# Kernel tuning notes

Measured on AMD Instinct MI355X. Metric: run time of the kernel, lower is better.

## Reference

```python
import jax, jax.numpy as jnp
import numpy as np

H = 128
N = 50000
E = 800000
VOCAB = 100
NUM_EDGE_BLOCKS = 4
NUM_UPD_BLOCKS = 2


def setup_inputs() -> dict:
    key = jax.random.key(0)
    ks = jax.random.split(key, 30)
    s = H ** -0.5
    nrm = lambda k, shp, sc: (jax.random.normal(k, shp, dtype=jnp.float32) * sc)
    inp = {
        'atom_num': jax.random.randint(ks[0], (N,), 0, VOCAB),
        'dis1': jax.random.uniform(ks[1], (E, 1), dtype=jnp.float32),
        'dis2': jax.random.uniform(ks[2], (E, 1), dtype=jnp.float32),
        'id1u': jax.random.randint(ks[3], (E,), 0, N),
        'id1v': jax.random.randint(ks[4], (E,), 0, N),
        'id2u': jax.random.randint(ks[5], (E,), 0, N),
        'id2v': jax.random.randint(ks[6], (E,), 0, N),
        # atom embedding table
        'emb': nrm(ks[7], (VOCAB, H), 1.0),
        # 4 edge-embedding blocks (edge_emb1, edge_emb2, update_edge1, update_edge2)
        'Wu': nrm(ks[8], (NUM_EDGE_BLOCKS, H, H), s),
        'Wv': nrm(ks[9], (NUM_EDGE_BLOCKS, H, H), s),
        'Wdis': nrm(ks[10], (NUM_EDGE_BLOCKS, 1, H), 1.0),
        'eb1': jnp.zeros((NUM_EDGE_BLOCKS, H), jnp.float32),
        'eW2': nrm(ks[11], (NUM_EDGE_BLOCKS, H, H), s),
        'eb2': jnp.zeros((NUM_EDGE_BLOCKS, H), jnp.float32),
        'eW3': nrm(ks[12], (NUM_EDGE_BLOCKS, H, H), s),
        'eb3': jnp.zeros((NUM_EDGE_BLOCKS, H), jnp.float32),
        # 2 atom-update blocks
        'Wh': nrm(ks[13], (NUM_UPD_BLOCKS, H, H), s),
        'Wa1': nrm(ks[14], (NUM_UPD_BLOCKS, H, H), s),
        'Wa2': nrm(ks[15], (NUM_UPD_BLOCKS, H, H), s),
        'ub1': jnp.zeros((NUM_UPD_BLOCKS, H), jnp.float32),
        'uW2': nrm(ks[16], (NUM_UPD_BLOCKS, H, H), s),
        'ub2': jnp.zeros((NUM_UPD_BLOCKS, H), jnp.float32),
        # output head
        'outW': nrm(ks[17], (H, 3), s),
        'outb': jnp.zeros((3,), jnp.float32),
    }
    return inp


def _edge_block(h, u, v, dis, Wu, Wv, Wdis, b1, W2, b2, W3, b3):
    # gather endpoint features, fuse with distance embedding, 3-layer MLP
    pre = h[u] @ Wu + h[v] @ Wv + dis @ Wdis + b1  # [E,H]
    t = jax.nn.silu(pre)
    t = jax.nn.silu(t @ W2 + b2)
    return t @ W3 + b3  # [E,H]


def _atom_update(h, m1, m2, id1u, id1v, id2u, id2v, Wh, Wa1, Wa2, b1, W2, b2):
    n = h.shape[0]
    a1 = jax.ops.segment_sum(m1, id1u, num_segments=n) + jax.ops.segment_sum(m1, id1v, num_segments=n)
    a2 = jax.ops.segment_sum(m2, id2u, num_segments=n) + jax.ops.segment_sum(m2, id2v, num_segments=n)
    t = jax.nn.silu(h @ Wh + a1 @ Wa1 + a2 @ Wa2 + b1)
    return h + t @ W2 + b2


def reference(atom_num, dis1, dis2, id1u, id1v, id2u, id2v, emb, Wu, Wv, Wdis, eb1, eW2, eb2, eW3, eb3, Wh, Wa1, Wa2, ub1, uW2, ub2, outW, outb):
    eblk = lambda i, h, u, v, d: _edge_block(h, u, v, d, Wu[i], Wv[i], Wdis[i], eb1[i], eW2[i], eb2[i], eW3[i], eb3[i])
    ablk = lambda j, h, m1, m2: _atom_update(h, m1, m2, id1u, id1v, id2u, id2v, Wh[j], Wa1[j], Wa2[j], ub1[j], uW2[j], ub2[j])
    h = emb[atom_num]  # [N,H]
    m1 = eblk(0, h, id1u, id1v, dis1)
    m2 = eblk(1, h, id2u, id2v, dis2)
    h = ablk(0, h, m1, m2)
    m1 = eblk(2, h, id1u, id1v, dis1)
    m2 = eblk(3, h, id2u, id2v, dis2)
    h = ablk(1, h, m1, m2)
    return h @ outW + outb  # [N,3]
```

## Files before the change

### kernel.cpp

```cpp
#include <hip/hip_runtime.h>

#define H 128
#define NATOM 50000
#define NEDGE 800000
#define CE (NEDGE / 2)

typedef __attribute__((ext_vector_type(8))) short short8;
typedef __attribute__((ext_vector_type(4))) float f32x4;
typedef __attribute__((ext_vector_type(4))) unsigned int uint4n;

#define MFMA16(a, b, c) __builtin_amdgcn_mfma_f32_16x16x32_bf16((a), (b), (c), 0, 0, 0)

__device__ __forceinline__ unsigned short f2b(float f) {
  unsigned int u = __float_as_uint(f);
  unsigned int r = (u + 0x7FFFu + ((u >> 16) & 1u)) >> 16;
  return (unsigned short)r;
}
__device__ __forceinline__ float b2f(unsigned short b) {
  return __uint_as_float(((unsigned int)b) << 16);
}

#if __has_builtin(__builtin_amdgcn_cvt_pk_bf16_f32)
__device__ __forceinline__ unsigned int f2b2(float lo, float hi) {
  typedef __bf16 bf16x2 __attribute__((ext_vector_type(2)));
  bf16x2 r = __builtin_amdgcn_cvt_pk_bf16_f32(lo, hi);
  union { bf16x2 v; unsigned int u; } c;
  c.v = r;
  return c.u;
}
#else
__device__ __forceinline__ unsigned int f2b2(float lo, float hi) {
  return (unsigned int)f2b(lo) | ((unsigned int)f2b(hi) << 16);
}
#endif

__device__ __forceinline__ float silu_f(float x) {
  return x * __builtin_amdgcn_rcpf(1.0f + __expf(-x));
}

struct PackSrc { const float* p[24]; };

__global__ void repack_kernel(PackSrc ps, unsigned short* __restrict__ dst) {
  const float* src = ps.p[blockIdx.x];
  unsigned short* d = dst + (size_t)blockIdx.x * 16384;
  for (int s = threadIdx.x; s < 2048; s += 256) {
    const int ct = s >> 8;
    const int kc = (s >> 6) & 3;
    const int lane = s & 63;
    const int r0 = kc * 32 + (lane >> 4) * 8;
    const int col = ct * 16 + (lane & 15);
    uint4 u;
    u.x = f2b2(src[(r0 + 0) * H + col], src[(r0 + 1) * H + col]);
    u.y = f2b2(src[(r0 + 2) * H + col], src[(r0 + 3) * H + col]);
    u.z = f2b2(src[(r0 + 4) * H + col], src[(r0 + 5) * H + col]);
    u.w = f2b2(src[(r0 + 6) * H + col], src[(r0 + 7) * H + col]);
    *(uint4*)(d + s * 8) = u;
  }
}

__global__ void embed_kernel(const int* __restrict__ atom_num, const float* __restrict__ emb,
                             unsigned short* __restrict__ h0) {
  const int idx = blockIdx.x * 256 + threadIdx.x;
  const int n = idx >> 6;
  const int c = (idx & 63) * 2;
  const float* src = emb + (size_t)atom_num[n] * H + c;
  *(unsigned int*)(h0 + (size_t)n * H + c) = f2b2(src[0], src[1]);
}

__global__ void zero_int_kernel(int4* __restrict__ p, int n4) {
  const int i = blockIdx.x * 256 + threadIdx.x;
  if (i < n4) p[i] = make_int4(0, 0, 0, 0);
}

__global__ void count_kernel(const int* __restrict__ u1, const int* __restrict__ v1,
                             const int* __restrict__ u2, const int* __restrict__ v2,
                             int* __restrict__ degU, int* __restrict__ degV) {
  const int e = blockIdx.x * 256 + threadIdx.x;
  atomicAdd(degU + u1[e], 1);
  atomicAdd(degU + NATOM + u2[e], 1);
  atomicAdd(degV + v1[e], 1);
  atomicAdd(degV + NATOM + v2[e], 1);
}

__global__ void scan_phase1(const int* __restrict__ deg, int* __restrict__ partials,
                            int ncells) {
  __shared__ int sh[256];
  const int t = threadIdx.x;
  const int base = blockIdx.x * 1024 + t * 4;
  int s = 0;
#pragma unroll
  for (int j = 0; j < 4; ++j) { const int i = base + j; if (i < ncells) s += deg[i]; }
  sh[t] = s;
  __syncthreads();
  for (int off = 128; off > 0; off >>= 1) {
    if (t < off) sh[t] += sh[t + off];
    __syncthreads();
  }
  if (t == 0) partials[blockIdx.x] = sh[0];
}

__global__ void scan_phase2(int* __restrict__ partials, int np) {
  __shared__ int sh[1024];
  const int t = threadIdx.x;
  const int v = t < np ? partials[t] : 0;
  sh[t] = v;
  __syncthreads();
  for (int off = 1; off < 1024; off <<= 1) {
    int x = 0;
    if (t >= off) x = sh[t - off];
    __syncthreads();
    sh[t] += x;
    __syncthreads();
  }
  if (t < np) partials[t] = sh[t] - v;
}

__global__ void scan_phase3(const int* __restrict__ deg, const int* __restrict__ partials,
                            int* __restrict__ start, int* __restrict__ cursor, int ncells) {
  __shared__ int sh[256];
  const int t = threadIdx.x;
  const int base = blockIdx.x * 1024 + t * 4;
  int v[4];
  int s = 0;
#pragma unroll
  for (int j = 0; j < 4; ++j) {
    const int i = base + j;
    v[j] = (i < ncells) ? deg[i] : 0;
    s += v[j];
  }
  sh[t] = s;
  __syncthreads();
  const int own = s;
  for (int off = 1; off < 256; off <<= 1) {
    int x = 0;
    if (t >= off) x = sh[t - off];
    __syncthreads();
    sh[t] += x;
    __syncthreads();
  }
  int o = partials[blockIdx.x] + sh[t] - own;
#pragma unroll
  for (int j = 0; j < 4; ++j) {
    const int i = base + j;
    if (i < ncells) {
      start[i] = o;
      cursor[i] = o;
      o += v[j];
      if (i == ncells - 1) start[ncells] = o;
    }
  }
}

__global__ void fill_fused_kernel(const int* __restrict__ u1, const int* __restrict__ v1,
                                  const float* __restrict__ dis1,
                                  const int* __restrict__ u2, const int* __restrict__ v2,
                                  const float* __restrict__ dis2,
                                  int* __restrict__ curU, int* __restrict__ curV,
                                  unsigned int* __restrict__ uvS,
                                  float* __restrict__ disS, int* __restrict__ listV,
                                  int npass) {
  const int apb = (NATOM + npass - 1) / npass;
  for (int p = 0; p < npass; ++p) {
    const int lo = p * apb, hi = lo + apb;
    for (int e = blockIdx.x * 256 + threadIdx.x; e < NEDGE; e += gridDim.x * 256) {
      int a = __builtin_nontemporal_load(u1 + e);
      if (a >= lo && a < hi) {
        const int v = __builtin_nontemporal_load(v1 + e);
        const int su = atomicAdd(curU + a, 1);
        uvS[su] = (unsigned int)a | ((unsigned int)v << 16);
        disS[su] = __builtin_nontemporal_load(dis1 + e);
        const int sv = atomicAdd(curV + v, 1);
        listV[sv] = su;
      }
      a = __builtin_nontemporal_load(u2 + e);
      if (a >= lo && a < hi) {
        const int v = __builtin_nontemporal_load(v2 + e);
        const int su = atomicAdd(curU + NATOM + a, 1);
        uvS[su] = (unsigned int)a | ((unsigned int)v << 16);
        disS[su] = __builtin_nontemporal_load(dis2 + e);
        const int sv = atomicAdd(curV + NATOM + v, 1);
        listV[sv] = su;
      }
    }
  }
}

__global__ __launch_bounds__(256, 2)
void pre_kernel(const unsigned short* __restrict__ h,
                const unsigned short* __restrict__ pWu, const unsigned short* __restrict__ pWv,
                unsigned short* __restrict__ hu, unsigned short* __restrict__ hv) {
  __shared__ __attribute__((aligned(16))) unsigned short sH[64][136];
  __shared__ __attribute__((aligned(16))) unsigned short sO[64][136];

  const int tid = threadIdx.x;
  const int wave = tid >> 6;
  const int lane = tid & 63;
  const int l15 = lane & 15;
  const int quad = lane >> 4;
  const int r0 = tid >> 4;
  const int ch = tid & 15;

  short8 wU[2][4], wV[2][4];
#pragma unroll
  for (int ct = 0; ct < 2; ++ct) {
#pragma unroll
    for (int kc = 0; kc < 4; ++kc) {
      const int off = (((wave * 2 + ct) * 4 + kc) * 64 + lane) * 8;
      wU[ct][kc] = *(const short8*)(pWu + off);
      wV[ct][kc] = *(const short8*)(pWv + off);
    }
  }

  const int n0 = blockIdx.x * 64;
#pragma unroll
  for (int it = 0; it < 4; ++it) {
    const int r = r0 + it * 16;
    int g = n0 + r; if (g >= NATOM) g = NATOM - 1;
    *(uint4*)(&sH[r][ch * 8]) = *(const uint4*)(h + (size_t)g * H + ch * 8);
  }
  __syncthreads();

  f32x4 au[4][2], av[4][2];
#pragma unroll
  for (int rt = 0; rt < 4; ++rt)
#pragma unroll
    for (int ct = 0; ct < 2; ++ct) {
      au[rt][ct] = (f32x4){0.f, 0.f, 0.f, 0.f};
      av[rt][ct] = (f32x4){0.f, 0.f, 0.f, 0.f};
    }
#pragma unroll
  for (int kc = 0; kc < 4; ++kc) {
#pragma unroll
    for (int rt = 0; rt < 4; ++rt) {
      const short8 a = *(const short8*)(&sH[rt * 16 + l15][kc * 32 + quad * 8]);
#pragma unroll
      for (int ct = 0; ct < 2; ++ct) {
        au[rt][ct] = MFMA16(a, wU[ct][kc], au[rt][ct]);
        av[rt][ct] = MFMA16(a, wV[ct][kc], av[rt][ct]);
      }
    }
  }
  __syncthreads();

#pragma unroll
  for (int rt = 0; rt < 4; ++rt) {
#pragma unroll
    for (int ct = 0; ct < 2; ++ct) {
      const int col = wave * 32 + ct * 16 + l15;
#pragma unroll
      for (int r = 0; r < 4; r += 2) {
        const int row = rt * 16 + quad * 4 + r;
        const unsigned int p = f2b2(au[rt][ct][r], au[rt][ct][r + 1]);
        sO[row][col] = (unsigned short)p;
        sO[row + 1][col] = (unsigned short)(p >> 16);
      }
    }
  }
  __syncthreads();
#pragma unroll
  for (int it = 0; it < 4; ++it) {
    const int r = r0 + it * 16;
    const int g = n0 + r;
    if (g < NATOM)
      *(uint4*)(hu + (size_t)g * H + ch * 8) = *(const uint4*)(&sO[r][ch * 8]);
  }
  __syncthreads();

#pragma unroll
  for (int rt = 0; rt < 4; ++rt) {
#pragma unroll
    for (int ct = 0; ct < 2; ++ct) {
      const int col = wave * 32 + ct * 16 + l15;
#pragma unroll
      for (int r = 0; r < 4; r += 2) {
        const int row = rt * 16 + quad * 4 + r;
        const unsigned int p = f2b2(av[rt][ct][r], av[rt][ct][r + 1]);
        sO[row][col] = (unsigned short)p;
        sO[row + 1][col] = (unsigned short)(p >> 16);
      }
    }
  }
  __syncthreads();
#pragma unroll
  for (int it = 0; it < 4; ++it) {
    const int r = r0 + it * 16;
    const int g = n0 + r;
    if (g < NATOM)
      *(uint4*)(hv + (size_t)g * H + ch * 8) = *(const uint4*)(&sO[r][ch * 8]);
  }
}

__global__ __launch_bounds__(256, 3)
void edge_kernel(const unsigned short* __restrict__ hu,
                 const unsigned short* __restrict__ hv,
                 const unsigned int* __restrict__ uv,
                 const float* __restrict__ dis,
                 const unsigned short* __restrict__ pW2, const unsigned short* __restrict__ pW3,
                 const float* __restrict__ Wdis, const float* __restrict__ bb1,
                 const float* __restrict__ bb2, const float* __restrict__ bb3,
                 unsigned short* __restrict__ msg, int eBase, int nTiles) {
  __shared__ __attribute__((aligned(16))) unsigned short sA[64][136];
  __shared__ __attribute__((aligned(16))) unsigned short sB[64][136];

  const int tid = threadIdx.x;
  const int wave = tid >> 6;
  const int lane = tid & 63;
  const int l15 = lane & 15;
  const int quad = lane >> 4;
  const int r0 = tid >> 4;
  const int ch = tid & 15;

  short8 wW2[2][4], wW3[2][4];
#pragma unroll
  for (int ct = 0; ct < 2; ++ct) {
#pragma unroll
    for (int kc = 0; kc < 4; ++kc) {
      const int off = (((wave * 2 + ct) * 4 + kc) * 64 + lane) * 8;
      wW2[ct][kc] = *(const short8*)(pW2 + off);
      wW3[ct][kc] = *(const short8*)(pW3 + off);
    }
  }
  float wd8[8], b18[8];
#pragma unroll
  for (int k = 0; k < 8; ++k) { wd8[k] = Wdis[ch * 8 + k]; b18[k] = bb1[ch * 8 + k]; }
  float vb2[2], vb3[2];
#pragma unroll
  for (int ct = 0; ct < 2; ++ct) {
    const int col = wave * 32 + ct * 16 + l15;
    vb2[ct] = bb2[col]; vb3[ct] = bb3[col];
  }

  const int stride = gridDim.x;
  int tile = blockIdx.x;

  uint4 pfU[4], pfV[4];
  float pfD[4];
  if (tile < nTiles) {
    const int e0 = eBase + tile * 64;
#pragma unroll
    for (int it = 0; it < 4; ++it) {
      const int e = e0 + r0 + it * 16;
      const unsigned int p = uv[e];
      pfU[it] = *(const uint4*)(hu + (size_t)(p & 0xFFFFu) * H + ch * 8);
      pfV[it] = *(const uint4*)(hv + (size_t)(p >> 16) * H + ch * 8);
      pfD[it] = dis[e];
    }
  }

  for (; tile < nTiles; tile += stride) {
#pragma unroll
    for (int it = 0; it < 4; ++it) {
      const int rr = r0 + it * 16;
      const float d = pfD[it];
      const unsigned int ua[4] = {pfU[it].x, pfU[it].y, pfU[it].z, pfU[it].w};
      const unsigned int va[4] = {pfV[it].x, pfV[it].y, pfV[it].z, pfV[it].w};
#pragma unroll
      for (int j = 0; j < 4; ++j) {
        const float x0 = b2f((unsigned short)ua[j]) + b2f((unsigned short)va[j]) +
                         d * wd8[2 * j] + b18[2 * j];
        const float x1 = b2f((unsigned short)(ua[j] >> 16)) + b2f((unsigned short)(va[j] >> 16)) +
                         d * wd8[2 * j + 1] + b18[2 * j + 1];
        *(unsigned int*)(&sA[rr][ch * 8 + 2 * j]) = f2b2(silu_f(x0), silu_f(x1));
      }
    }
    const int tileN = tile + stride;
    if (tileN < nTiles) {
      const int e0n = eBase + tileN * 64;
#pragma unroll
      for (int it = 0; it < 4; ++it) {
        const int e = e0n + r0 + it * 16;
        const unsigned int p = uv[e];
        pfU[it] = *(const uint4*)(hu + (size_t)(p & 0xFFFFu) * H + ch * 8);
        pfV[it] = *(const uint4*)(hv + (size_t)(p >> 16) * H + ch * 8);
        pfD[it] = dis[e];
      }
    }
    __syncthreads();

    f32x4 acc[4][2];
#pragma unroll
    for (int rt = 0; rt < 4; ++rt)
#pragma unroll
      for (int ct = 0; ct < 2; ++ct) acc[rt][ct] = (f32x4){0.f, 0.f, 0.f, 0.f};
#pragma unroll
    for (int kc = 0; kc < 4; ++kc) {
#pragma unroll
      for (int rt = 0; rt < 4; ++rt) {
        const short8 a = *(const short8*)(&sA[rt * 16 + l15][kc * 32 + quad * 8]);
#pragma unroll
        for (int ct = 0; ct < 2; ++ct) acc[rt][ct] = MFMA16(a, wW2[ct][kc], acc[rt][ct]);
      }
    }
#pragma unroll
    for (int rt = 0; rt < 4; ++rt) {
#pragma unroll
      for (int ct = 0; ct < 2; ++ct) {
        const int col = wave * 32 + ct * 16 + l15;
#pragma unroll
        for (int r = 0; r < 4; r += 2) {
          const int row = rt * 16 + quad * 4 + r;
          const unsigned int p = f2b2(silu_f(acc[rt][ct][r] + vb2[ct]),
                                      silu_f(acc[rt][ct][r + 1] + vb2[ct]));
          sB[row][col] = (unsigned short)p;
          sB[row + 1][col] = (unsigned short)(p >> 16);
        }
      }
    }
    __syncthreads();

#pragma unroll
    for (int rt = 0; rt < 4; ++rt)
#pragma unroll
      for (int ct = 0; ct < 2; ++ct) acc[rt][ct] = (f32x4){0.f, 0.f, 0.f, 0.f};
#pragma unroll
    for (int kc = 0; kc < 4; ++kc) {
#pragma unroll
      for (int rt = 0; rt < 4; ++rt) {
        const short8 a = *(const short8*)(&sB[rt * 16 + l15][kc * 32 + quad * 8]);
#pragma unroll
        for (int ct = 0; ct < 2; ++ct) acc[rt][ct] = MFMA16(a, wW3[ct][kc], acc[rt][ct]);
      }
    }
#pragma unroll
    for (int rt = 0; rt < 4; ++rt) {
#pragma unroll
      for (int ct = 0; ct < 2; ++ct) {
        const int col = wave * 32 + ct * 16 + l15;
#pragma unroll
        for (int r = 0; r < 4; r += 2) {
          const int row = rt * 16 + quad * 4 + r;
          const unsigned int p = f2b2(acc[rt][ct][r] + vb3[ct],
                                      acc[rt][ct][r + 1] + vb3[ct]);
          sA[row][col] = (unsigned short)p;
          sA[row + 1][col] = (unsigned short)(p >> 16);
        }
      }
    }
    __syncthreads();
#pragma unroll
    for (int it = 0; it < 4; ++it) {
      const int rr = r0 + it * 16;
      __builtin_nontemporal_store(*(const uint4n*)(&sA[rr][ch * 8]),
                                  (uint4n*)(msg + (size_t)(tile * 64 + rr) * H + ch * 8));
    }
    __syncthreads();
  }
}

__global__ __launch_bounds__(256)
void aggregate_kernel(const int* __restrict__ startU, const int* __restrict__ startV,
                      const int* __restrict__ listV,
                      const unsigned short* __restrict__ msg, int chunkBase, int cellBase,
                      float* __restrict__ af32, unsigned short* __restrict__ aout,
                      int isFirst, int isLast) {
  const int atom = blockIdx.x * 4 + (threadIdx.x >> 6);
  const int lane = threadIdx.x & 63;
  float ax = 0.f, ay = 0.f;
  if (!isFirst) {
    const float2 p = *(const float2*)(af32 + (size_t)atom * H + lane * 2);
    ax = p.x; ay = p.y;
  }
  const unsigned int* mp = (const unsigned int*)msg;

  const int gsu = startU[cellBase + atom];
  const int geu = startU[cellBase + atom + 1];
  int lo = gsu > chunkBase ? gsu : chunkBase;
  int hi = geu < chunkBase + CE ? geu : chunkBase + CE;
  int p = lo - chunkBase;
  const int pe = hi - chunkBase;
  for (; p + 3 < pe; p += 4) {
    unsigned int u[4];
#pragma unroll
    for (int j = 0; j < 4; ++j) u[j] = mp[(size_t)(p + j) * 64 + lane];
#pragma unroll
    for (int j = 0; j < 4; ++j) {
      ax += b2f((unsigned short)u[j]);
      ay += b2f((unsigned short)(u[j] >> 16));
    }
  }
  for (; p < pe; ++p) {
    const unsigned int u0 = mp[(size_t)p * 64 + lane];
    ax += b2f((unsigned short)u0);
    ay += b2f((unsigned short)(u0 >> 16));
  }

  const int sv = startV[cellBase + atom];
  const int ev = startV[cellBase + atom + 1];
  int i = sv;
  for (; i + 7 < ev; i += 8) {
    unsigned int d[8];
#pragma unroll
    for (int j = 0; j < 8; ++j)
      d[j] = (unsigned int)(__builtin_nontemporal_load(listV + i + j) - chunkBase);
    unsigned int u[8];
#pragma unroll
    for (int j = 0; j < 8; ++j) {
      u[j] = 0u;
      if (d[j] < (unsigned int)CE)
        u[j] = __builtin_nontemporal_load(mp + (size_t)d[j] * 64 + lane);
    }
#pragma unroll
    for (int j = 0; j < 8; ++j) {
      ax += b2f((unsigned short)u[j]);
      ay += b2f((unsigned short)(u[j] >> 16));
    }
  }
  for (; i < ev; ++i) {
    const unsigned int d = (unsigned int)(__builtin_nontemporal_load(listV + i) - chunkBase);
    if (d < (unsigned int)CE) {
      const unsigned int u0 = __builtin_nontemporal_load(mp + (size_t)d * 64 + lane);
      ax += b2f((unsigned short)u0);
      ay += b2f((unsigned short)(u0 >> 16));
    }
  }

  if (isLast) {
    *(unsigned int*)(aout + (size_t)atom * H + lane * 2) = f2b2(ax, ay);
  } else {
    *(float2*)(af32 + (size_t)atom * H + lane * 2) = make_float2(ax, ay);
  }
}

__global__ __launch_bounds__(256, 2)
void update_kernel(const unsigned short* __restrict__ hin,
                   const unsigned short* __restrict__ a1, const unsigned short* __restrict__ a2,
                   const unsigned short* __restrict__ pWh, const unsigned short* __restrict__ pWa1,
                   const unsigned short* __restrict__ pWa2, const unsigned short* __restrict__ pWo,
                   const float* __restrict__ b1, const float* __restrict__ b2,
                   unsigned short* __restrict__ hout) {
  __shared__ __attribute__((aligned(16))) unsigned short sH[64][136];
  __shared__ __attribute__((aligned(16))) unsigned short s1[64][136];
  __shared__ __attribute__((aligned(16))) unsigned short s2[64][136];

  const int tid = threadIdx.x;
  const int wave = tid >> 6;
  const int lane = tid & 63;
  const int l15 = lane & 15;
  const int quad = lane >> 4;

  short8 wWh[2][4], wW1[2][4], wW2m[2][4], wWo[2][4];
#pragma unroll
  for (int ct = 0; ct < 2; ++ct) {
#pragma unroll
    for (int kc = 0; kc < 4; ++kc) {
      const int off = (((wave * 2 + ct) * 4 + kc) * 64 + lane) * 8;
      wWh[ct][kc] = *(const short8*)(pWh + off);
      wW1[ct][kc] = *(const short8*)(pWa1 + off);
      wW2m[ct][kc] = *(const short8*)(pWa2 + off);
      wWo[ct][kc] = *(const short8*)(pWo + off);
    }
  }
  float vb1[2], vb2[2];
#pragma unroll
  for (int ct = 0; ct < 2; ++ct) {
    const int col = wave * 32 + ct * 16 + l15;
    vb1[ct] = b1[col]; vb2[ct] = b2[col];
  }

  const int n0 = blockIdx.x * 64;
#pragma unroll
  for (int it = 0; it < 4; ++it) {
    const int r = (tid >> 4) + it * 16;
    const int ch = tid & 15;
    int g = n0 + r; if (g >= NATOM) g = NATOM - 1;
    *(uint4*)(&sH[r][ch * 8]) = *(const uint4*)(hin + (size_t)g * H + ch * 8);
    *(uint4*)(&s1[r][ch * 8]) = *(const uint4*)(a1 + (size_t)g * H + ch * 8);
    *(uint4*)(&s2[r][ch * 8]) = *(const uint4*)(a2 + (size_t)g * H + ch * 8);
  }
  __syncthreads();

  f32x4 acc[4][2];
#pragma unroll
  for (int rt = 0; rt < 4; ++rt)
#pragma unroll
    for (int ct = 0; ct < 2; ++ct) acc[rt][ct] = (f32x4){0.f, 0.f, 0.f, 0.f};

#pragma unroll
  for (int kc = 0; kc < 4; ++kc) {
#pragma unroll
    for (int rt = 0; rt < 4; ++rt) {
      const short8 ah = *(const short8*)(&sH[rt * 16 + l15][kc * 32 + quad * 8]);
      const short8 aa1 = *(const short8*)(&s1[rt * 16 + l15][kc * 32 + quad * 8]);
      const short8 aa2 = *(const short8*)(&s2[rt * 16 + l15][kc * 32 + quad * 8]);
#pragma unroll
      for (int ct = 0; ct < 2; ++ct) {
        acc[rt][ct] = MFMA16(ah, wWh[ct][kc], acc[rt][ct]);
        acc[rt][ct] = MFMA16(aa1, wW1[ct][kc], acc[rt][ct]);
        acc[rt][ct] = MFMA16(aa2, wW2m[ct][kc], acc[rt][ct]);
      }
    }
  }
  __syncthreads();

#pragma unroll
  for (int rt = 0; rt < 4; ++rt) {
#pragma unroll
    for (int ct = 0; ct < 2; ++ct) {
      const int col = wave * 32 + ct * 16 + l15;
#pragma unroll
      for (int r = 0; r < 4; r += 2) {
        const int row = rt * 16 + quad * 4 + r;
        const unsigned int p = f2b2(silu_f(acc[rt][ct][r] + vb1[ct]),
                                    silu_f(acc[rt][ct][r + 1] + vb1[ct]));
        s1[row][col] = (unsigned short)p;
        s1[row + 1][col] = (unsigned short)(p >> 16);
      }
    }
  }
  __syncthreads();

#pragma unroll
  for (int rt = 0; rt < 4; ++rt)
#pragma unroll
    for (int ct = 0; ct < 2; ++ct) acc[rt][ct] = (f32x4){0.f, 0.f, 0.f, 0.f};
#pragma unroll
  for (int kc = 0; kc < 4; ++kc) {
#pragma unroll
    for (int rt = 0; rt < 4; ++rt) {
      const short8 a = *(const short8*)(&s1[rt * 16 + l15][kc * 32 + quad * 8]);
#pragma unroll
      for (int ct = 0; ct < 2; ++ct) acc[rt][ct] = MFMA16(a, wWo[ct][kc], acc[rt][ct]);
    }
  }
  __syncthreads();
#pragma unroll
  for (int rt = 0; rt < 4; ++rt) {
#pragma unroll
    for (int ct = 0; ct < 2; ++ct) {
      const int col = wave * 32 + ct * 16 + l15;
#pragma unroll
      for (int r = 0; r < 4; r += 2) {
        const int row = rt * 16 + quad * 4 + r;
        const float v0 = b2f(sH[row][col]) + acc[rt][ct][r] + vb2[ct];
        const float v1 = b2f(sH[row + 1][col]) + acc[rt][ct][r + 1] + vb2[ct];
        const unsigned int p = f2b2(v0, v1);
        s2[row][col] = (unsigned short)p;
        s2[row + 1][col] = (unsigned short)(p >> 16);
      }
    }
  }
  __syncthreads();
#pragma unroll
  for (int it = 0; it < 4; ++it) {
    const int r = (tid >> 4) + it * 16;
    const int ch = tid & 15;
    const int g = n0 + r;
    if (g < NATOM)
      *(uint4*)(hout + (size_t)g * H + ch * 8) = *(const uint4*)(&s2[r][ch * 8]);
  }
}

__global__ void out_kernel(const unsigned short* __restrict__ h,
                           const float* __restrict__ outW, const float* __restrict__ outb,
                           float* __restrict__ out) {
  const int atom = blockIdx.x * 4 + (threadIdx.x >> 6);
  const int lane = threadIdx.x & 63;
  float s0 = 0.f, s1 = 0.f, s2 = 0.f;
#pragma unroll
  for (int kk = 0; kk < 2; ++kk) {
    const int k = lane + kk * 64;
    const float hv = b2f(h[(size_t)atom * H + k]);
    s0 += hv * outW[k * 3 + 0];
    s1 += hv * outW[k * 3 + 1];
    s2 += hv * outW[k * 3 + 2];
  }
#pragma unroll
  for (int off = 32; off > 0; off >>= 1) {
    s0 += __shfl_down(s0, off);
    s1 += __shfl_down(s1, off);
    s2 += __shfl_down(s2, off);
  }
  if (lane == 0) {
    out[atom * 3 + 0] = s0 + outb[0];
    out[atom * 3 + 1] = s1 + outb[1];
    out[atom * 3 + 2] = s2 + outb[2];
  }
}

extern "C" void kernel_launch(void* const* d_in, const int* in_sizes, int n_in,
                              void* d_out, int out_size, void* d_ws, size_t ws_size,
                              hipStream_t stream) {
  const int* atom_num = (const int*)d_in[0];
  const float* dis1 = (const float*)d_in[1];
  const float* dis2 = (const float*)d_in[2];
  const int* id1u = (const int*)d_in[3];
  const int* id1v = (const int*)d_in[4];
  const int* id2u = (const int*)d_in[5];
  const int* id2v = (const int*)d_in[6];
  const float* emb = (const float*)d_in[7];
  const float* Wu = (const float*)d_in[8];
  const float* Wv = (const float*)d_in[9];
  const float* Wdis = (const float*)d_in[10];
  const float* eb1 = (const float*)d_in[11];
  const float* eW2 = (const float*)d_in[12];
  const float* eb2 = (const float*)d_in[13];
  const float* eW3 = (const float*)d_in[14];
  const float* eb3 = (const float*)d_in[15];
  const float* Wh = (const float*)d_in[16];
  const float* Wa1 = (const float*)d_in[17];
  const float* Wa2 = (const float*)d_in[18];
  const float* ub1 = (const float*)d_in[19];
  const float* uW2 = (const float*)d_in[20];
  const float* ub2 = (const float*)d_in[21];
  const float* outW = (const float*)d_in[22];
  const float* outb = (const float*)d_in[23];

  auto pad = [](size_t x) { return (x + 255) & ~(size_t)255; };
  const int N2 = 2 * NATOM;
  const int nparts = (N2 + 1023) / 1024;

  char* ws = (char*)d_ws;
  size_t off = 0;
  auto take = [&](size_t bytes) { char* p = ws + off; off += pad(bytes); return p; };
  unsigned short* pw   = (unsigned short*)take(786432);
  unsigned short* h0   = (unsigned short*)take((size_t)NATOM * H * 2);
  unsigned short* a1   = (unsigned short*)take((size_t)NATOM * H * 2);
  unsigned short* a2   = (unsigned short*)take((size_t)NATOM * H * 2);
  unsigned short* hu   = (unsigned short*)take((size_t)NATOM * H * 2);
  unsigned short* hv   = (unsigned short*)take((size_t)NATOM * H * 2);
  unsigned int* uvS    = (unsigned int*)take((size_t)2 * NEDGE * 4);
  float* disS          = (float*)take((size_t)2 * NEDGE * 4);
  int* listV           = (int*)take((size_t)2 * NEDGE * 4);
  int* startU          = (int*)take(((size_t)N2 + 1) * 4);
  int* startV          = (int*)take(((size_t)N2 + 1) * 4);
  float* af32          = (float*)take((size_t)NATOM * H * 4);
  char* ovlRegion      = ws + off;
  unsigned short* msg  = (unsigned short*)ovlRegion;
  int* degU            = (int*)ovlRegion;
  int* degV            = degU + N2;
  int* curU            = degV + N2;
  int* curV            = curU + N2;
  int* partU           = curV + N2;
  int* partV           = partU + 1024;

  PackSrc ps;
  for (int i = 0; i < 4; ++i) {
    ps.p[i] = Wu + i * 16384;
    ps.p[4 + i] = Wv + i * 16384;
    ps.p[8 + i] = eW2 + i * 16384;
    ps.p[12 + i] = eW3 + i * 16384;
  }
  for (int j = 0; j < 2; ++j) {
    ps.p[16 + j] = Wh + j * 16384;
    ps.p[18 + j] = Wa1 + j * 16384;
    ps.p[20 + j] = Wa2 + j * 16384;
    ps.p[22 + j] = uW2 + j * 16384;
  }
  repack_kernel<<<24, 256, 0, stream>>>(ps, pw);
  embed_kernel<<<12500, 256, 0, stream>>>(atom_num, emb, h0);

  {
    const int n4 = (int)(((size_t)2 * N2 * 4 + 15) / 16);
    zero_int_kernel<<<(n4 + 255) / 256, 256, 0, stream>>>((int4*)degU, n4);
    count_kernel<<<NEDGE / 256, 256, 0, stream>>>(id1u, id1v, id2u, id2v, degU, degV);
    scan_phase1<<<nparts, 256, 0, stream>>>(degU, partU, N2);
    scan_phase2<<<1, 1024, 0, stream>>>(partU, nparts);
    scan_phase3<<<nparts, 256, 0, stream>>>(degU, partU, startU, curU, N2);
    scan_phase1<<<nparts, 256, 0, stream>>>(degV, partV, N2);
    scan_phase2<<<1, 1024, 0, stream>>>(partV, nparts);
    scan_phase3<<<nparts, 256, 0, stream>>>(degV, partV, startV, curV, N2);
    fill_fused_kernel<<<1024, 256, 0, stream>>>(id1u, id1v, dis1, id2u, id2v, dis2,
                                                curU, curV, uvS, disS, listV, 8);
  }

  const int upd_grid = (NATOM + 63) / 64;
  const int AGG_GRID = NATOM / 4;
  const int tilesPerChunk = CE / 64;
  const int EDGE_GRID = tilesPerChunk < 768 ? tilesPerChunk : 768;

  const unsigned short* pWu_[4] = {pw, pw + 16384, pw + 2 * 16384, pw + 3 * 16384};
  const unsigned short* pWv_[4] = {pw + 4 * 16384, pw + 5 * 16384, pw + 6 * 16384, pw + 7 * 16384};
  const unsigned short* pW2_[4] = {pw + 8 * 16384, pw + 9 * 16384, pw + 10 * 16384, pw + 11 * 16384};
  const unsigned short* pW3_[4] = {pw + 12 * 16384, pw + 13 * 16384, pw + 14 * 16384, pw + 15 * 16384};

  for (int layer = 0; layer < 2; ++layer) {
    for (int set = 0; set < 2; ++set) {
      const int blk = layer * 2 + set;
      unsigned short* aout = set == 0 ? a1 : a2;
      pre_kernel<<<upd_grid, 256, 0, stream>>>(h0, pWu_[blk], pWv_[blk], hu, hv);
      for (int c = 0; c < 2; ++c) {
        const int chunkBase = set * NEDGE + c * CE;
        edge_kernel<<<EDGE_GRID, 256, 0, stream>>>(hu, hv, uvS, disS,
            pW2_[blk], pW3_[blk],
            Wdis + blk * H, eb1 + blk * H, eb2 + blk * H, eb3 + blk * H,
            msg, chunkBase, tilesPerChunk);
        aggregate_kernel<<<AGG_GRID, 256, 0, stream>>>(startU, startV, listV, msg,
            chunkBase, set * NATOM, af32, aout, c == 0 ? 1 : 0, c == 1 ? 1 : 0);
      }
    }
    update_kernel<<<upd_grid, 256, 0, stream>>>(h0, a1, a2,
        pw + (16 + layer) * 16384, pw + (18 + layer) * 16384,
        pw + (20 + layer) * 16384, pw + (22 + layer) * 16384,
        ub1 + layer * H, ub2 + layer * H, h0);
  }

  out_kernel<<<12500, 256, 0, stream>>>(h0, outW, outb, (float*)d_out);
}
```

Before: 1.626 ms.

## Store edge messages as FP8 and aggregate each edge set in one pass

Edge messages are now packed from bf16 to FP8 e4m3 before they are written, which halves the message buffer. That lets a whole 800k-edge set fit in the workspace, so the two-chunk split is removed. Each set now runs one edge kernel and one aggregate kernel, and the fp32 partial-sum buffer and its extra read/write pass are gone. The risk is lower message precision, since e4m3 has a 3-bit mantissa and saturates at 448, which may hurt accuracy.

```diff
diff --git a/kernel.cpp b/kernel.cpp
--- a/kernel.cpp
+++ b/kernel.cpp
@@ -3,11 +3,11 @@
 #define H 128
 #define NATOM 50000
 #define NEDGE 800000
-#define CE (NEDGE / 2)
 
 typedef __attribute__((ext_vector_type(8))) short short8;
 typedef __attribute__((ext_vector_type(4))) float f32x4;
-typedef __attribute__((ext_vector_type(4))) unsigned int uint4n;
+typedef __attribute__((ext_vector_type(2))) float f32x2;
+typedef __attribute__((ext_vector_type(2))) unsigned int uint2n;
 
 #define MFMA16(a, b, c) __builtin_amdgcn_mfma_f32_16x16x32_bf16((a), (b), (c), 0, 0, 0)
 
@@ -33,6 +33,68 @@
   return (unsigned int)f2b(lo) | ((unsigned int)f2b(hi) << 16);
 }
 #endif
+
+#if __has_builtin(__builtin_amdgcn_cvt_pk_fp8_f32) && __has_builtin(__builtin_amdgcn_cvt_pk_f32_fp8)
+#define HW_FP8 1
+#else
+#define HW_FP8 0
+#endif
+
+#if !HW_FP8
+__device__ __forceinline__ unsigned int enc_e4m3(float f) {
+  unsigned int b = __float_as_uint(f);
+  unsigned int s = (b >> 31) << 7;
+  float a = fabsf(f);
+  if (a >= 448.f) return s | 0x7Eu;
+  if (a < 0.015625f) {
+    int m = (int)(a * 512.f + 0.5f);
+    if (m > 7) m = 7;
+    return s | (unsigned int)m;
+  }
+  unsigned int ab = b & 0x7FFFFFFFu;
+  unsigned int r = ab + 0x7FFFFu + ((ab >> 20) & 1u);
+  unsigned int e = (r >> 23) - 127u + 7u;
+  unsigned int m = (r >> 20) & 7u;
+  if (e >= 16u) { e = 15u; m = 6u; }
+  return s | (e << 3) | m;
+}
+__device__ __forceinline__ float dec_e4m3(unsigned int c) {
+  unsigned int s = (c >> 7) & 1u, e = (c >> 3) & 15u, m = c & 7u;
+  float v = (e == 0) ? (float)m * 0.001953125f
+                     : __uint_as_float(((e - 7u + 127u) << 23) | (m << 20));
+  return s ? -v : v;
+}
+#endif
+
+__device__ __forceinline__ void pack8_fp8(const unsigned int w[4], unsigned int out[2]) {
+  float f[8];
+#pragma unroll
+  for (int j = 0; j < 4; ++j) {
+    f[2 * j] = b2f((unsigned short)w[j]);
+    f[2 * j + 1] = b2f((unsigned short)(w[j] >> 16));
+  }
+#if HW_FP8
+  int w0 = __builtin_amdgcn_cvt_pk_fp8_f32(f[0], f[1], 0, false);
+  w0 = __builtin_amdgcn_cvt_pk_fp8_f32(f[2], f[3], w0, true);
+  int w1 = __builtin_amdgcn_cvt_pk_fp8_f32(f[4], f[5], 0, false);
+  w1 = __builtin_amdgcn_cvt_pk_fp8_f32(f[6], f[7], w1, true);
+  out[0] = (unsigned int)w0;
+  out[1] = (unsigned int)w1;
+#else
+  out[0] = enc_e4m3(f[0]) | (enc_e4m3(f[1]) << 8) | (enc_e4m3(f[2]) << 16) | (enc_e4m3(f[3]) << 24);
+  out[1] = enc_e4m3(f[4]) | (enc_e4m3(f[5]) << 8) | (enc_e4m3(f[6]) << 16) | (enc_e4m3(f[7]) << 24);
+#endif
+}
+
+__device__ __forceinline__ void unpack2_fp8(unsigned short s, float& x, float& y) {
+#if HW_FP8
+  f32x2 v = __builtin_amdgcn_cvt_pk_f32_fp8((int)(unsigned int)s, false);
+  x = v[0]; y = v[1];
+#else
+  x = dec_e4m3(s & 0xFFu);
+  y = dec_e4m3((s >> 8) & 0xFFu);
+#endif
+}
 
 __device__ __forceinline__ float silu_f(float x) {
   return x * __builtin_amdgcn_rcpf(1.0f + __expf(-x));
@@ -298,7 +360,7 @@
                  const unsigned short* __restrict__ pW2, const unsigned short* __restrict__ pW3,
                  const float* __restrict__ Wdis, const float* __restrict__ bb1,
                  const float* __restrict__ bb2, const float* __restrict__ bb3,
-                 unsigned short* __restrict__ msg, int eBase, int nTiles) {
+                 unsigned char* __restrict__ msg, int eBase, int nTiles) {
   __shared__ __attribute__((aligned(16))) unsigned short sA[64][136];
   __shared__ __attribute__((aligned(16))) unsigned short sB[64][136];
 
@@ -440,8 +502,12 @@
 #pragma unroll
     for (int it = 0; it < 4; ++it) {
       const int rr = r0 + it * 16;
-      __builtin_nontemporal_store(*(const uint4n*)(&sA[rr][ch * 8]),
-                                  (uint4n*)(msg + (size_t)(tile * 64 + rr) * H + ch * 8));
+      unsigned int w[4], o[2];
+      *(uint4*)w = *(const uint4*)(&sA[rr][ch * 8]);
+      pack8_fp8(w, o);
+      uint2n ov; ov.x = o[0]; ov.y = o[1];
+      __builtin_nontemporal_store(ov,
+          (uint2n*)(msg + (size_t)(tile * 64 + rr) * H + ch * 8));
     }
     __syncthreads();
   }
@@ -450,75 +516,58 @@
 __global__ __launch_bounds__(256)
 void aggregate_kernel(const int* __restrict__ startU, const int* __restrict__ startV,
                       const int* __restrict__ listV,
-                      const unsigned short* __restrict__ msg, int chunkBase, int cellBase,
-                      float* __restrict__ af32, unsigned short* __restrict__ aout,
-                      int isFirst, int isLast) {
+                      const unsigned char* __restrict__ msg, int eBase, int cellBase,
+                      unsigned short* __restrict__ aout) {
   const int atom = blockIdx.x * 4 + (threadIdx.x >> 6);
   const int lane = threadIdx.x & 63;
-  float ax = 0.f, ay = 0.f;
-  if (!isFirst) {
-    const float2 p = *(const float2*)(af32 + (size_t)atom * H + lane * 2);
-    ax = p.x; ay = p.y;
-  }
-  const unsigned int* mp = (const unsigned int*)msg;
-
-  const int gsu = startU[cellBase + atom];
-  const int geu = startU[cellBase + atom + 1];
-  int lo = gsu > chunkBase ? gsu : chunkBase;
-  int hi = geu < chunkBase + CE ? geu : chunkBase + CE;
-  int p = lo - chunkBase;
-  const int pe = hi - chunkBase;
-  for (; p + 3 < pe; p += 4) {
-    unsigned int u[4];
-#pragma unroll
-    for (int j = 0; j < 4; ++j) u[j] = mp[(size_t)(p + j) * 64 + lane];
-#pragma unroll
-    for (int j = 0; j < 4; ++j) {
-      ax += b2f((unsigned short)u[j]);
-      ay += b2f((unsigned short)(u[j] >> 16));
-    }
-  }
-  for (; p < pe; ++p) {
-    const unsigned int u0 = mp[(size_t)p * 64 + lane];
-    ax += b2f((unsigned short)u0);
-    ay += b2f((unsigned short)(u0 >> 16));
-  }
-
+  const int su = startU[cellBase + atom] - eBase;
+  const int eu = startU[cellBase + atom + 1] - eBase;
   const int sv = startV[cellBase + atom];
   const int ev = startV[cellBase + atom + 1];
+  float ax = 0.f, ay = 0.f;
+  const unsigned char* mp = msg + lane * 2;
+
+  int p = su;
+  for (; p + 3 < eu; p += 4) {
+    unsigned short s[4];
+#pragma unroll
+    for (int j = 0; j < 4; ++j) s[j] = *(const unsigned short*)(mp + (size_t)(p + j) * H);
+#pragma unroll
+    for (int j = 0; j < 4; ++j) {
+      float x, y; unpack2_fp8(s[j], x, y);
+      ax += x; ay += y;
+    }
+  }
+  for (; p < eu; ++p) {
+    const unsigned short s0 = *(const unsigned short*)(mp + (size_t)p * H);
+    float x, y; unpack2_fp8(s0, x, y);
+    ax += x; ay += y;
+  }
+
   int i = sv;
   for (; i + 7 < ev; i += 8) {
-    unsigned int d[8];
+    int r[8];
+#pragma unroll
+    for (int j = 0; j < 8; ++j) r[j] = __builtin_nontemporal_load(listV + i + j) - eBase;
+    unsigned short s[8];
 #pragma unroll
     for (int j = 0; j < 8; ++j)
-      d[j] = (unsigned int)(__builtin_nontemporal_load(listV + i + j) - chunkBase);
-    unsigned int u[8];
+      s[j] = __builtin_nontemporal_load((const unsigned short*)(mp + (size_t)r[j] * H));
 #pragma unroll
     for (int j = 0; j < 8; ++j) {
-      u[j] = 0u;
-      if (d[j] < (unsigned int)CE)
-        u[j] = __builtin_nontemporal_load(mp + (size_t)d[j] * 64 + lane);
-    }
-#pragma unroll
-    for (int j = 0; j < 8; ++j) {
-      ax += b2f((unsigned short)u[j]);
-      ay += b2f((unsigned short)(u[j] >> 16));
+      float x, y; unpack2_fp8(s[j], x, y);
+      ax += x; ay += y;
     }
   }
   for (; i < ev; ++i) {
-    const unsigned int d = (unsigned int)(__builtin_nontemporal_load(listV + i) - chunkBase);
-    if (d < (unsigned int)CE) {
-      const unsigned int u0 = __builtin_nontemporal_load(mp + (size_t)d * 64 + lane);
-      ax += b2f((unsigned short)u0);
-      ay += b2f((unsigned short)(u0 >> 16));
-    }
-  }
-
-  if (isLast) {
-    *(unsigned int*)(aout + (size_t)atom * H + lane * 2) = f2b2(ax, ay);
-  } else {
-    *(float2*)(af32 + (size_t)atom * H + lane * 2) = make_float2(ax, ay);
-  }
+    const int r = __builtin_nontemporal_load(listV + i) - eBase;
+    const unsigned short s0 =
+        __builtin_nontemporal_load((const unsigned short*)(mp + (size_t)r * H));
+    float x, y; unpack2_fp8(s0, x, y);
+    ax += x; ay += y;
+  }
+
+  *(unsigned int*)(aout + (size_t)atom * H + lane * 2) = f2b2(ax, ay);
 }
 
 __global__ __launch_bounds__(256, 2)
@@ -723,9 +772,8 @@
   int* listV           = (int*)take((size_t)2 * NEDGE * 4);
   int* startU          = (int*)take(((size_t)N2 + 1) * 4);
   int* startV          = (int*)take(((size_t)N2 + 1) * 4);
-  float* af32          = (float*)take((size_t)NATOM * H * 4);
   char* ovlRegion      = ws + off;
-  unsigned short* msg  = (unsigned short*)ovlRegion;
+  unsigned char* msg   = (unsigned char*)ovlRegion;
   int* degU            = (int*)ovlRegion;
   int* degV            = degU + N2;
   int* curU            = degV + N2;
@@ -765,8 +813,8 @@
 
   const int upd_grid = (NATOM + 63) / 64;
   const int AGG_GRID = NATOM / 4;
-  const int tilesPerChunk = CE / 64;
-  const int EDGE_GRID = tilesPerChunk < 768 ? tilesPerChunk : 768;
+  const int nTiles = NEDGE / 64;
+  const int EDGE_GRID = 768;
 
   const unsigned short* pWu_[4] = {pw, pw + 16384, pw + 2 * 16384, pw + 3 * 16384};
   const unsigned short* pWv_[4] = {pw + 4 * 16384, pw + 5 * 16384, pw + 6 * 16384, pw + 7 * 16384};
@@ -776,17 +824,16 @@
   for (int layer = 0; layer < 2; ++layer) {
     for (int set = 0; set < 2; ++set) {
       const int blk = layer * 2 + set;
+      const int eBase = set * NEDGE;
+      const int cellBase = set * NATOM;
       unsigned short* aout = set == 0 ? a1 : a2;
       pre_kernel<<<upd_grid, 256, 0, stream>>>(h0, pWu_[blk], pWv_[blk], hu, hv);
-      for (int c = 0; c < 2; ++c) {
-        const int chunkBase = set * NEDGE + c * CE;
-        edge_kernel<<<EDGE_GRID, 256, 0, stream>>>(hu, hv, uvS, disS,
-            pW2_[blk], pW3_[blk],
-            Wdis + blk * H, eb1 + blk * H, eb2 + blk * H, eb3 + blk * H,
-            msg, chunkBase, tilesPerChunk);
-        aggregate_kernel<<<AGG_GRID, 256, 0, stream>>>(startU, startV, listV, msg,
-            chunkBase, set * NATOM, af32, aout, c == 0 ? 1 : 0, c == 1 ? 1 : 0);
-      }
+      edge_kernel<<<EDGE_GRID, 256, 0, stream>>>(hu, hv, uvS, disS,
+          pW2_[blk], pW3_[blk],
+          Wdis + blk * H, eb1 + blk * H, eb2 + blk * H, eb3 + blk * H,
+          msg, eBase, nTiles);
+      aggregate_kernel<<<AGG_GRID, 256, 0, stream>>>(startU, startV, listV, msg,
+          eBase, cellBase, aout);
     }
     update_kernel<<<upd_grid, 256, 0, stream>>>(h0, a1, a2,
         pw + (16 + layer) * 16384, pw + (18 + layer) * 16384,
```

Result: faster. 1.437 ms (-11.6%).
